# Performance work log

Hardware: AMD Instinct MI355X
Metric: run time of the kernel (lower is better)

The kernel has to match this reference:

```python
import jax, jax.numpy as jnp
import numpy as np

B, S, D, H = 4, 1024, 1024, 16
E = 8                 # num_experts
FF1 = 4096            # d_hidden * expansion_factor * 2 (swiglu in)
FF2 = 2048            # d_hidden * expansion_factor (swiglu out / linear2 in)
TEMP = 0.5            # gating temperature
RMS_EPS_GATE = float(np.finfo(np.float32).eps)  # torch RMSNorm default eps
NORM_EPS = 1e-8       # layer_norm_eps


def setup_inputs() -> dict:
    key = jax.random.key(0)
    ks = jax.random.split(key, 8)
    s = 0.02
    return {
        "x": jax.random.normal(ks[0], (B, S, D), jnp.float32),
        "w_qkv": jax.random.normal(ks[1], (3 * D, D), jnp.float32) * s,
        "w_out": jax.random.normal(ks[2], (D, D), jnp.float32) * s,
        "norm1_w": jnp.ones((D,), jnp.float32),
        "norm2_w": jnp.ones((D,), jnp.float32),
        "gate_w": jax.random.normal(ks[3], (E, D), jnp.float32) * s,
        "gate_b": jnp.zeros((E,), jnp.float32),
        "gate_rms_w": jnp.ones((E,), jnp.float32),
        "w1": jax.random.normal(ks[4], (E, D, FF1), jnp.float32) * s,
        "w2": jax.random.normal(ks[5], (E, FF2, D), jnp.float32) * s,
    }


def _rmsnorm(x, w, eps):
    return x * w * jax.lax.rsqrt(jnp.mean(x * x, axis=-1, keepdims=True) + eps)


def _attn(h, w_qkv, w_out):
    qkv = h @ w_qkv.T                              # [B,S,3D]
    q, k, v = jnp.split(qkv, 3, axis=-1)
    dh = D // H
    q = q.reshape(B, S, H, dh)
    k = k.reshape(B, S, H, dh)
    v = v.reshape(B, S, H, dh)
    scores = jnp.einsum("bqhd,bkhd->bhqk", q, k) / jnp.sqrt(jnp.float32(dh))
    p = jax.nn.softmax(scores, axis=-1)
    o = jnp.einsum("bhqk,bkhd->bqhd", p, v).reshape(B, S, D)
    return o @ w_out.T


def _moe(h, gate_w, gate_b, gate_rms_w, w1, w2):
    xf = h.reshape(-1, D)                          # [N,D]
    logits = _rmsnorm(xf @ gate_w.T + gate_b, gate_rms_w, RMS_EPS_GATE)
    gates = jax.nn.softmax(logits / TEMP, axis=-1)  # [N,E]
    top_g, _ = jax.lax.top_k(gates, 1)              # top_k = 1
    # capacity dispatch mask degenerates to all-ones (capacity >= 1), so
    # normalized gate = g / (g + 1e-6)
    g = top_g[:, 0] / (top_g[:, 0] + 1e-6)          # [N]
    h1 = jnp.einsum("nd,edf->nef", xf, w1)          # [N,E,FF1]
    a, b = jnp.split(h1, 2, axis=-1)                # SwiGLU
    act = a * jax.nn.silu(b)                        # [N,E,FF2]
    outs = jnp.einsum("nef,efd->ned", act, w2)      # [N,E,D]
    # gate broadcasts over the expert axis (as in the original code)
    comb = outs.sum(axis=1) * g[:, None]
    return comb.reshape(h.shape)


def reference(x, w_qkv, w_out, norm1_w, norm2_w, gate_w, gate_b, gate_rms_w, w1, w2):
    # pre-norm transformer block, eval mode (no dropout / gating noise)
    x = x + _attn(_rmsnorm(x, norm1_w, NORM_EPS), w_qkv, w_out)
    x = x + _moe(_rmsnorm(x, norm2_w, NORM_EPS), gate_w, gate_b, gate_rms_w, w1, w2)
    return x
```

## Files before the change

kernel.cpp:

```cpp
#include <hip/hip_runtime.h>
#include <hip/hip_bf16.h>
#include <math.h>

typedef __bf16 bf16_t;
typedef __bf16 bf16x8 __attribute__((ext_vector_type(8)));
typedef float f32x4 __attribute__((ext_vector_type(4)));

typedef const __attribute__((address_space(1))) void* gptr_t;
typedef __attribute__((address_space(3))) void* lptr_t;

#define MFMA16(a, b, c) __builtin_amdgcn_mfma_f32_16x16x32_bf16((a), (b), (c), 0, 0, 0)
#define BAR() __builtin_amdgcn_s_barrier()
#define WAIT_LGKM()                                        \
  do {                                                     \
    asm volatile("s_waitcnt lgkmcnt(0)" ::: "memory");     \
    __builtin_amdgcn_sched_barrier(0);                     \
  } while (0)
#define WAIT_VM4()                                         \
  do {                                                     \
    asm volatile("s_waitcnt vmcnt(4)" ::: "memory");       \
    __builtin_amdgcn_sched_barrier(0);                     \
  } while (0)
#define WAIT_VM8()                                         \
  do {                                                     \
    asm volatile("s_waitcnt vmcnt(8)" ::: "memory");       \
    __builtin_amdgcn_sched_barrier(0);                     \
  } while (0)
#define WAIT_VM0()                                         \
  do {                                                     \
    asm volatile("s_waitcnt vmcnt(0)" ::: "memory");       \
    __builtin_amdgcn_sched_barrier(0);                     \
  } while (0)

__device__ __forceinline__ void gload_lds16(const bf16_t* g, bf16_t* l) {
  __builtin_amdgcn_global_load_lds((gptr_t)g, (lptr_t)l, 16, 0, 0);
}

__global__ __launch_bounds__(256) void conv_kernel(const float* __restrict__ in,
                                                   bf16_t* __restrict__ out, int n4) {
  int i = blockIdx.x * 256 + threadIdx.x;
  if (i >= n4) return;
  float4 v = ((const float4*)in)[i];
  bf16_t* o = out + (size_t)i * 4;
  o[0] = (bf16_t)v.x; o[1] = (bf16_t)v.y; o[2] = (bf16_t)v.z; o[3] = (bf16_t)v.w;
}

__global__ __launch_bounds__(256) void transp_w1(const float* __restrict__ in,
                                                 bf16_t* __restrict__ out) {
  __shared__ float tile[32][33];
  const float* ip = in + (size_t)blockIdx.z * 1024 * 4096;
  bf16_t* op = out + (size_t)blockIdx.z * 4096 * 1024;
  int tx = threadIdx.x, ty = threadIdx.y;
  int r0 = blockIdx.y * 32, c0 = blockIdx.x * 32;
#pragma unroll
  for (int i = 0; i < 32; i += 8)
    tile[ty + i][tx] = ip[(size_t)(r0 + ty + i) * 4096 + c0 + tx];
  __syncthreads();
#pragma unroll
  for (int i = 0; i < 32; i += 8) {
    int c = c0 + ty + i;
    int p = (c < 2048) ? ((c >> 5) * 64 + (c & 31))
                       : (((c - 2048) >> 5) * 64 + 32 + ((c - 2048) & 31));
    op[(size_t)p * 1024 + r0 + tx] = (bf16_t)tile[tx][ty + i];
  }
}

__global__ __launch_bounds__(256) void transp_w2(const float* __restrict__ in,
                                                 bf16_t* __restrict__ out) {
  __shared__ float tile[32][33];
  const float* ip = in + (size_t)blockIdx.z * 2048 * 1024;
  int tx = threadIdx.x, ty = threadIdx.y;
  int r0 = blockIdx.y * 32, c0 = blockIdx.x * 32;
#pragma unroll
  for (int i = 0; i < 32; i += 8)
    tile[ty + i][tx] = ip[(size_t)(r0 + ty + i) * 1024 + c0 + tx];
  __syncthreads();
#pragma unroll
  for (int i = 0; i < 32; i += 8)
    out[(size_t)(c0 + ty + i) * 16384 + blockIdx.z * 2048 + r0 + tx] = (bf16_t)tile[tx][ty + i];
}

__global__ __launch_bounds__(256) void rmsnorm_kernel(const float* __restrict__ x,
                                                      const float* __restrict__ w,
                                                      bf16_t* __restrict__ out, float eps) {
  int row = blockIdx.x;
  int t = threadIdx.x;
  const float4* xr = (const float4*)(x + (size_t)row * 1024);
  float4 v = xr[t];
  float ss = v.x * v.x + v.y * v.y + v.z * v.z + v.w * v.w;
#pragma unroll
  for (int off = 1; off < 64; off <<= 1) ss += __shfl_xor(ss, off, 64);
  __shared__ float red[4];
  int wave = t >> 6, lane = t & 63;
  if (lane == 0) red[wave] = ss;
  __syncthreads();
  ss = red[0] + red[1] + red[2] + red[3];
  float inv = rsqrtf(ss * (1.0f / 1024.0f) + eps);
  float4 wv = ((const float4*)w)[t];
  bf16_t* o = out + (size_t)row * 1024 + t * 4;
  o[0] = (bf16_t)(v.x * wv.x * inv);
  o[1] = (bf16_t)(v.y * wv.y * inv);
  o[2] = (bf16_t)(v.z * wv.z * inv);
  o[3] = (bf16_t)(v.w * wv.w * inv);
}

template <int EPI>
__global__ __launch_bounds__(512, 2) void gemm256(const bf16_t* __restrict__ A,
                                                  const bf16_t* __restrict__ Bt,
                                                  void* __restrict__ C,
                                                  const float* __restrict__ resid,
                                                  int M, int N, int K, int lda, int ldb) {
  __shared__ bf16_t As[2][256 * 64];
  __shared__ bf16_t Bs[2][256 * 64];
  const int tid = threadIdx.x;
  const int wave = tid >> 6, lane = tid & 63;

  const int gx = gridDim.x, gy = gridDim.y;
  int nwg = gx * gy * gridDim.z;
  int lin = blockIdx.x + gx * (blockIdx.y + gy * blockIdx.z);
  int wid = ((nwg & 7) == 0) ? ((lin & 7) * (nwg >> 3) + (lin >> 3)) : lin;
  const int bx = wid % gx;
  const int by = (wid / gx) % gy;
  const int bz = wid / (gx * gy);

  const int m0 = by * 256, n0 = bx * 256;
  const int wr = (wave >> 2) * 128, wc = (wave & 3) * 64;
  const int fr = lane & 15, fq = lane >> 4;

  if (EPI == 4) Bt += (size_t)bz * 4096 * 1024;
  if (EPI == 5) {
    A += (size_t)bz * K;
    Bt += (size_t)bz * K;
  }

  const int srw = lane >> 3;
  const int sgc = (lane & 7) ^ srw;
  const bf16_t* aBase = A + (size_t)(m0 + wave * 8 + srw) * lda + sgc * 8;
  const bf16_t* bBase = Bt + (size_t)(n0 + wave * 8 + srw) * ldb + sgc * 8;

  auto stageA = [&](bf16_t* buf, int kt) {
#pragma unroll
    for (int i = 0; i < 4; ++i) {
      int r = i * 64;
      gload_lds16(aBase + (size_t)r * lda + kt * 64, &buf[(r + wave * 8) * 64]);
    }
  };
  auto stageB = [&](bf16_t* buf, int kt) {
#pragma unroll
    for (int i = 0; i < 4; ++i) {
      int r = i * 64;
      gload_lds16(bBase + (size_t)r * ldb + kt * 64, &buf[(r + wave * 8) * 64]);
    }
  };

  f32x4 acc[8][4] = {};
  bf16x8 a_[4][2], b_[4][2];

  auto readA = [&](int b, int mh) {
#pragma unroll
    for (int q = 0; q < 4; ++q)
#pragma unroll
      for (int ks = 0; ks < 2; ++ks) {
        int r = wr + mh * 64 + q * 16 + fr;
        a_[q][ks] = *(const bf16x8*)&As[b][r * 64 + (((fq + ks * 4) ^ (fr & 7)) << 3)];
      }
  };
  auto readB = [&](int b, int nh) {
#pragma unroll
    for (int q = 0; q < 2; ++q)
#pragma unroll
      for (int ks = 0; ks < 2; ++ks) {
        int r = wc + nh * 32 + q * 16 + fr;
        b_[nh * 2 + q][ks] = *(const bf16x8*)&Bs[b][r * 64 + (((fq + ks * 4) ^ (fr & 7)) << 3)];
      }
  };
  auto mfma16x = [&](int mh, int nh) {
    __builtin_amdgcn_s_setprio(1);
#pragma unroll
    for (int q = 0; q < 4; ++q)
#pragma unroll
      for (int n = 0; n < 2; ++n)
#pragma unroll
        for (int ks = 0; ks < 2; ++ks)
          acc[mh * 4 + q][nh * 2 + n] =
              MFMA16(a_[q][ks], b_[nh * 2 + n][ks], acc[mh * 4 + q][nh * 2 + n]);
    __builtin_amdgcn_s_setprio(0);
  };

  const int NKT = K >> 6;
  stageB(Bs[0], 0);
  stageA(As[0], 0);
  stageB(Bs[1], 1);
  stageA(As[1], 1);
  WAIT_VM8();
  BAR();
  readA(0, 0);
  readB(0, 0);

  for (int it = 0; it < (NKT >> 1) - 1; ++it) {
    const int t2 = 2 * it + 2, t3 = 2 * it + 3;
    WAIT_LGKM(); mfma16x(0, 0); readB(0, 1); BAR();
    WAIT_LGKM(); mfma16x(0, 1); readA(0, 1); BAR();
    WAIT_LGKM(); mfma16x(1, 0); stageB(Bs[0], t2); WAIT_VM4(); BAR();
    WAIT_LGKM(); mfma16x(1, 1); readA(1, 0); readB(1, 0); stageA(As[0], t2); BAR();
    WAIT_LGKM(); mfma16x(0, 0); readB(1, 1); BAR();
    WAIT_LGKM(); mfma16x(0, 1); readA(1, 1); BAR();
    WAIT_LGKM(); mfma16x(1, 0); stageB(Bs[1], t3); WAIT_VM4(); BAR();
    WAIT_LGKM(); mfma16x(1, 1); readA(0, 0); readB(0, 0); stageA(As[1], t3); BAR();
  }

  WAIT_LGKM(); mfma16x(0, 0); readB(0, 1); BAR();
  WAIT_LGKM(); mfma16x(0, 1); readA(0, 1); BAR();
  WAIT_LGKM(); mfma16x(1, 0); WAIT_VM0(); BAR();
  WAIT_LGKM(); mfma16x(1, 1); readA(1, 0); readB(1, 0); BAR();
  WAIT_LGKM(); mfma16x(0, 0); readB(1, 1); BAR();
  WAIT_LGKM(); mfma16x(0, 1); readA(1, 1); BAR();
  WAIT_LGKM(); mfma16x(1, 0); BAR();
  WAIT_LGKM(); mfma16x(1, 1);

  if (EPI == 4) {
    bf16_t* act = (bf16_t*)C;
    int strip = (n0 >> 6) + (wave & 3);
#pragma unroll
    for (int mq = 0; mq < 8; ++mq)
#pragma unroll
      for (int n = 0; n < 2; ++n)
#pragma unroll
        for (int j = 0; j < 4; ++j) {
          size_t row = (size_t)(m0 + wr + mq * 16 + fq * 4 + j);
          size_t col = (size_t)bz * 2048 + strip * 32 + n * 16 + fr;
          float a = acc[mq][n][j], b = acc[mq][n + 2][j];
          act[row * 16384 + col] = (bf16_t)(a * (b / (1.0f + __expf(-b))));
        }
    return;
  }
#pragma unroll
  for (int mq = 0; mq < 8; ++mq)
#pragma unroll
    for (int n = 0; n < 4; ++n)
#pragma unroll
      for (int j = 0; j < 4; ++j) {
        size_t row = (size_t)(m0 + wr + mq * 16 + fq * 4 + j);
        size_t col = (size_t)(n0 + wc + n * 16 + fr);
        float v = acc[mq][n][j];
        if (EPI == 0)
          ((bf16_t*)C)[row * N + col] = (bf16_t)v;
        else if (EPI == 1)
          ((float*)C)[row * N + col] = resid[row * N + col] + v;
        else if (EPI == 5)
          ((float*)C + (size_t)bz * M * N)[row * N + col] = v;
      }
}

__global__ __launch_bounds__(256) void attn_kernel(const bf16_t* __restrict__ qkv,
                                                   bf16_t* __restrict__ o) {
  const int S = 1024, LD = 3072;
  int qt = blockIdx.x, bh = blockIdx.y;
  int b = bh >> 4, h = bh & 15;
  int tid = threadIdx.x, wave = tid >> 6, lane = tid & 63;
  int fr = lane & 15, fq = lane >> 4, kg = fq * 8;
  int q0 = qt * 64 + wave * 16;
  const bf16_t* qb = qkv + (size_t)b * S * LD + h * 64;
  const bf16_t* kb = qb + 1024;
  const bf16_t* vb = qb + 2048;

  __shared__ bf16_t Ks[64 * 64];
  __shared__ bf16_t Vt[64 * 64];
  __shared__ bf16_t Ps[4][16 * 72];

  bf16x8 qf0 = *(const bf16x8*)&qb[(size_t)(q0 + fr) * LD + kg];
  bf16x8 qf1 = *(const bf16x8*)&qb[(size_t)(q0 + fr) * LD + 32 + kg];

  f32x4 acc[4] = {};
  float mrow[4] = {-1e30f, -1e30f, -1e30f, -1e30f};
  float ssum[4] = {0.f, 0.f, 0.f, 0.f};

  for (int k0 = 0; k0 < S; k0 += 64) {
#pragma unroll
    for (int cc = 0; cc < 2; ++cc) {
      int c = tid + cc * 256;
      int r = c >> 3, ch = c & 7;
      *(bf16x8*)&Ks[r * 64 + ((ch ^ (r & 7)) << 3)] =
          *(const bf16x8*)&kb[(size_t)(k0 + r) * LD + ch * 8];
      bf16x8 vv = *(const bf16x8*)&vb[(size_t)(k0 + r) * LD + ch * 8];
#pragma unroll
      for (int i = 0; i < 8; ++i) {
        int d = ch * 8 + i;
        int cs = ((r >> 3) ^ (d >> 3) ^ (d & 7)) & 7;
        Vt[d * 64 + cs * 8 + (r & 7)] = vv[i];
      }
    }
    __syncthreads();

    f32x4 s[4];
#pragma unroll
    for (int kc = 0; kc < 4; ++kc) {
      int row = kc * 16 + fr, sw = row & 7;
      bf16x8 kf0 = *(const bf16x8*)&Ks[row * 64 + ((fq ^ sw) << 3)];
      bf16x8 kf1 = *(const bf16x8*)&Ks[row * 64 + (((4 + fq) ^ sw) << 3)];
      f32x4 z = {};
      z = MFMA16(qf0, kf0, z);
      z = MFMA16(qf1, kf1, z);
      s[kc] = z * 0.125f;
    }
    float pmax[4], psum[4], scl[4];
#pragma unroll
    for (int j = 0; j < 4; ++j)
      pmax[j] = fmaxf(fmaxf(s[0][j], s[1][j]), fmaxf(s[2][j], s[3][j]));
#pragma unroll
    for (int off = 1; off < 16; off <<= 1)
#pragma unroll
      for (int j = 0; j < 4; ++j) pmax[j] = fmaxf(pmax[j], __shfl_xor(pmax[j], off, 64));
#pragma unroll
    for (int j = 0; j < 4; ++j) {
      float nm = fmaxf(mrow[j], pmax[j]);
      scl[j] = __expf(mrow[j] - nm);
      mrow[j] = nm;
      psum[j] = 0.f;
    }
#pragma unroll
    for (int kc = 0; kc < 4; ++kc)
#pragma unroll
      for (int j = 0; j < 4; ++j) {
        float p = __expf(s[kc][j] - mrow[j]);
        psum[j] += p;
        Ps[wave][(fq * 4 + j) * 72 + kc * 16 + fr] = (bf16_t)p;
      }
#pragma unroll
    for (int off = 1; off < 16; off <<= 1)
#pragma unroll
      for (int j = 0; j < 4; ++j) psum[j] += __shfl_xor(psum[j], off, 64);
#pragma unroll
    for (int j = 0; j < 4; ++j) ssum[j] = ssum[j] * scl[j] + psum[j];
#pragma unroll
    for (int n = 0; n < 4; ++n)
#pragma unroll
      for (int j = 0; j < 4; ++j) acc[n][j] *= scl[j];
    asm volatile("s_waitcnt lgkmcnt(0)" ::: "memory");
    bf16x8 pa[2];
#pragma unroll
    for (int ks = 0; ks < 2; ++ks) pa[ks] = *(const bf16x8*)&Ps[wave][fr * 72 + ks * 32 + kg];
#pragma unroll
    for (int n = 0; n < 4; ++n) {
      int d = n * 16 + fr;
      int swd = ((d >> 3) ^ (d & 7)) & 7;
#pragma unroll
      for (int ks = 0; ks < 2; ++ks) {
        bf16x8 vbf = *(const bf16x8*)&Vt[d * 64 + (((ks * 4 + fq) ^ swd) << 3)];
        acc[n] = MFMA16(pa[ks], vbf, acc[n]);
      }
    }
    __syncthreads();
  }
#pragma unroll
  for (int n = 0; n < 4; ++n)
#pragma unroll
    for (int j = 0; j < 4; ++j) {
      size_t row = (size_t)b * S + q0 + fq * 4 + j;
      o[row * 1024 + h * 64 + n * 16 + fr] = (bf16_t)(acc[n][j] / ssum[j]);
    }
}

__global__ __launch_bounds__(256) void gate_kernel(const bf16_t* __restrict__ hn,
                                                   const float* __restrict__ gw,
                                                   const float* __restrict__ gb,
                                                   const float* __restrict__ grms,
                                                   float* __restrict__ g) {
  int n = blockIdx.x * 4 + (threadIdx.x >> 6);
  int lane = threadIdx.x & 63;
  const bf16_t* xr = hn + (size_t)n * 1024;
  float acc[8] = {};
  for (int i = lane; i < 1024; i += 64) {
    float xv = (float)xr[i];
#pragma unroll
    for (int e = 0; e < 8; ++e) acc[e] += xv * gw[e * 1024 + i];
  }
#pragma unroll
  for (int e = 0; e < 8; ++e)
    for (int off = 1; off < 64; off <<= 1) acc[e] += __shfl_xor(acc[e], off, 64);
  float l[8], ms = 0.f;
#pragma unroll
  for (int e = 0; e < 8; ++e) {
    l[e] = acc[e] + gb[e];
    ms += l[e] * l[e];
  }
  float inv = rsqrtf(ms * 0.125f + 1.1920928955078125e-07f);
  float mx = -1e30f;
#pragma unroll
  for (int e = 0; e < 8; ++e) {
    l[e] = l[e] * inv * grms[e] * 2.0f;
    mx = fmaxf(mx, l[e]);
  }
  float s = 0.f;
#pragma unroll
  for (int e = 0; e < 8; ++e) s += __expf(l[e] - mx);
  float t = 1.0f / s;
  if (lane == 0) g[n] = t / (t + 1e-6f);
}

__global__ __launch_bounds__(256) void combine4(const float* __restrict__ moep,
                                                const float* __restrict__ x1,
                                                const float* __restrict__ g,
                                                float* __restrict__ out, int Mc) {
  size_t i4 = (size_t)blockIdx.x * 256 + threadIdx.x;
  size_t row = i4 >> 8;
  size_t stride4 = (size_t)Mc * 256;
  float4 s = {0.f, 0.f, 0.f, 0.f};
#pragma unroll
  for (int z = 0; z < 4; ++z) {
    float4 v = ((const float4*)moep)[z * stride4 + i4];
    s.x += v.x; s.y += v.y; s.z += v.z; s.w += v.w;
  }
  float gv = g[row];
  float4 xv = ((const float4*)x1)[i4];
  float4 r;
  r.x = xv.x + s.x * gv;
  r.y = xv.y + s.y * gv;
  r.z = xv.z + s.z * gv;
  r.w = xv.w + s.w * gv;
  ((float4*)out)[i4] = r;
}

extern "C" void kernel_launch(void* const* d_in, const int* in_sizes, int n_in,
                              void* d_out, int out_size, void* d_ws, size_t ws_size,
                              hipStream_t stream) {
  const float* x = (const float*)d_in[0];
  const float* w_qkv = (const float*)d_in[1];
  const float* w_out = (const float*)d_in[2];
  const float* norm1_w = (const float*)d_in[3];
  const float* norm2_w = (const float*)d_in[4];
  const float* gate_w = (const float*)d_in[5];
  const float* gate_b = (const float*)d_in[6];
  const float* gate_rms = (const float*)d_in[7];
  const float* w1 = (const float*)d_in[8];
  const float* w2 = (const float*)d_in[9];
  float* out = (float*)d_out;

  const size_t baseB = (8ull * 4096 * 1024 + 1024ull * 16384 + 3072ull * 1024 +
                        1024ull * 1024 + 4096ull * 1024) * 2 +
                       4096ull * 1024 * 4 + 4096 * 4;
  int cc = 4;
  if (ws_size >= baseB + 4096ull * 16384 * 2 + 4ull * 4096 * 1024 * 4)
    cc = 1;
  else if (ws_size >= baseB + 2048ull * 16384 * 2 + 4ull * 2048 * 1024 * 4)
    cc = 2;
  const int Mc = 4096 / cc;

  char* ws = (char*)d_ws;
  size_t off = 0;
  auto alloc = [&](size_t bytes) {
    char* p = ws + off;
    off += bytes;
    return p;
  };
  bf16_t* w1t = (bf16_t*)alloc(8ull * 4096 * 1024 * 2);
  bf16_t* w2t = (bf16_t*)alloc(1024ull * 16384 * 2);
  bf16_t* wqkvb = (bf16_t*)alloc(3072ull * 1024 * 2);
  bf16_t* woutb = (bf16_t*)alloc(1024ull * 1024 * 2);
  bf16_t* hn = (bf16_t*)alloc(4096ull * 1024 * 2);
  float* x1 = (float*)alloc(4096ull * 1024 * 4);
  float* gbuf = (float*)alloc(4096ull * 4);
  bf16_t* act = (bf16_t*)alloc((size_t)Mc * 16384 * 2);
  float* moep = (float*)alloc(4ull * Mc * 1024 * 4);
  bf16_t* qkvb = (bf16_t*)act;
  bf16_t* attno = (bf16_t*)moep;

  conv_kernel<<<3072, 256, 0, stream>>>(w_qkv, wqkvb, 3072 * 1024 / 4);
  conv_kernel<<<1024, 256, 0, stream>>>(w_out, woutb, 1024 * 1024 / 4);
  transp_w1<<<dim3(128, 32, 8), dim3(32, 8), 0, stream>>>(w1, w1t);
  transp_w2<<<dim3(32, 64, 8), dim3(32, 8), 0, stream>>>(w2, w2t);

  rmsnorm_kernel<<<4096, 256, 0, stream>>>(x, norm1_w, hn, 1e-8f);
  gemm256<0><<<dim3(12, 16), 512, 0, stream>>>(hn, wqkvb, qkvb, nullptr, 4096, 3072, 1024,
                                               1024, 1024);
  attn_kernel<<<dim3(16, 64), 256, 0, stream>>>(qkvb, attno);
  gemm256<1><<<dim3(4, 16), 512, 0, stream>>>(attno, woutb, x1, x, 4096, 1024, 1024, 1024,
                                              1024);

  rmsnorm_kernel<<<4096, 256, 0, stream>>>(x1, norm2_w, hn, 1e-8f);
  gate_kernel<<<1024, 256, 0, stream>>>(hn, gate_w, gate_b, gate_rms, gbuf);
  for (int c = 0; c < cc; ++c) {
    gemm256<4><<<dim3(16, Mc / 256, 8), 512, 0, stream>>>(
        hn + (size_t)c * Mc * 1024, w1t, act, nullptr, Mc, 4096, 1024, 1024, 1024);
    gemm256<5><<<dim3(4, Mc / 256, 4), 512, 0, stream>>>(
        act, w2t, moep, nullptr, Mc, 1024, 4096, 16384, 16384);
    combine4<<<Mc, 256, 0, stream>>>(moep, x1 + (size_t)c * Mc * 1024, gbuf + (size_t)c * Mc,
                                     out + (size_t)c * Mc * 1024, Mc);
  }
}
```

Measured before the change: 604.9 us.

## Restructure GEMM main loop into four phases with fewer barriers

Reorganizes the software-pipelined GEMM inner loop from eight barrier-separated phases to four. Each phase now issues two MFMA groups back to back, and s_setprio is raised around the combined group. Both B sub-tiles are read up front, and the A/B global stages are issued together with a vmcnt(8) wait. The aim is to cut barrier and lgkm wait overhead and to give longer uninterrupted MFMA bursts. In exchange, more LDS fragment reads are in flight at once, which raises register pressure, and load-compute interleaving becomes coarser.

```diff
diff --git a/kernel.cpp b/kernel.cpp
--- a/kernel.cpp
+++ b/kernel.cpp
@@ -14,11 +14,6 @@
 #define WAIT_LGKM()                                        \
   do {                                                     \
     asm volatile("s_waitcnt lgkmcnt(0)" ::: "memory");     \
-    __builtin_amdgcn_sched_barrier(0);                     \
-  } while (0)
-#define WAIT_VM4()                                         \
-  do {                                                     \
-    asm volatile("s_waitcnt vmcnt(4)" ::: "memory");       \
     __builtin_amdgcn_sched_barrier(0);                     \
   } while (0)
 #define WAIT_VM8()                                         \
@@ -175,7 +170,6 @@
       }
   };
   auto mfma16x = [&](int mh, int nh) {
-    __builtin_amdgcn_s_setprio(1);
 #pragma unroll
     for (int q = 0; q < 4; ++q)
 #pragma unroll
@@ -184,7 +178,6 @@
         for (int ks = 0; ks < 2; ++ks)
           acc[mh * 4 + q][nh * 2 + n] =
               MFMA16(a_[q][ks], b_[nh * 2 + n][ks], acc[mh * 4 + q][nh * 2 + n]);
-    __builtin_amdgcn_s_setprio(0);
   };
 
   const int NKT = K >> 6;
@@ -196,27 +189,71 @@
   BAR();
   readA(0, 0);
   readB(0, 0);
+  readB(0, 1);
 
   for (int it = 0; it < (NKT >> 1) - 1; ++it) {
     const int t2 = 2 * it + 2, t3 = 2 * it + 3;
-    WAIT_LGKM(); mfma16x(0, 0); readB(0, 1); BAR();
-    WAIT_LGKM(); mfma16x(0, 1); readA(0, 1); BAR();
-    WAIT_LGKM(); mfma16x(1, 0); stageB(Bs[0], t2); WAIT_VM4(); BAR();
-    WAIT_LGKM(); mfma16x(1, 1); readA(1, 0); readB(1, 0); stageA(As[0], t2); BAR();
-    WAIT_LGKM(); mfma16x(0, 0); readB(1, 1); BAR();
-    WAIT_LGKM(); mfma16x(0, 1); readA(1, 1); BAR();
-    WAIT_LGKM(); mfma16x(1, 0); stageB(Bs[1], t3); WAIT_VM4(); BAR();
-    WAIT_LGKM(); mfma16x(1, 1); readA(0, 0); readB(0, 0); stageA(As[1], t3); BAR();
-  }
-
-  WAIT_LGKM(); mfma16x(0, 0); readB(0, 1); BAR();
-  WAIT_LGKM(); mfma16x(0, 1); readA(0, 1); BAR();
-  WAIT_LGKM(); mfma16x(1, 0); WAIT_VM0(); BAR();
-  WAIT_LGKM(); mfma16x(1, 1); readA(1, 0); readB(1, 0); BAR();
-  WAIT_LGKM(); mfma16x(0, 0); readB(1, 1); BAR();
-  WAIT_LGKM(); mfma16x(0, 1); readA(1, 1); BAR();
-  WAIT_LGKM(); mfma16x(1, 0); BAR();
-  WAIT_LGKM(); mfma16x(1, 1);
+    WAIT_LGKM();
+    __builtin_amdgcn_s_setprio(1);
+    mfma16x(0, 0); mfma16x(0, 1);
+    __builtin_amdgcn_s_setprio(0);
+    readA(0, 1);
+    BAR();
+    WAIT_LGKM();
+    __builtin_amdgcn_s_setprio(1);
+    mfma16x(1, 0); mfma16x(1, 1);
+    __builtin_amdgcn_s_setprio(0);
+    stageB(Bs[0], t2);
+    stageA(As[0], t2);
+    WAIT_VM8();
+    readA(1, 0);
+    readB(1, 0);
+    readB(1, 1);
+    BAR();
+    WAIT_LGKM();
+    __builtin_amdgcn_s_setprio(1);
+    mfma16x(0, 0); mfma16x(0, 1);
+    __builtin_amdgcn_s_setprio(0);
+    readA(1, 1);
+    BAR();
+    WAIT_LGKM();
+    __builtin_amdgcn_s_setprio(1);
+    mfma16x(1, 0); mfma16x(1, 1);
+    __builtin_amdgcn_s_setprio(0);
+    stageB(Bs[1], t3);
+    stageA(As[1], t3);
+    WAIT_VM8();
+    readA(0, 0);
+    readB(0, 0);
+    readB(0, 1);
+    BAR();
+  }
+
+  WAIT_LGKM();
+  __builtin_amdgcn_s_setprio(1);
+  mfma16x(0, 0); mfma16x(0, 1);
+  __builtin_amdgcn_s_setprio(0);
+  readA(0, 1);
+  BAR();
+  WAIT_LGKM();
+  __builtin_amdgcn_s_setprio(1);
+  mfma16x(1, 0); mfma16x(1, 1);
+  __builtin_amdgcn_s_setprio(0);
+  WAIT_VM0();
+  readA(1, 0);
+  readB(1, 0);
+  readB(1, 1);
+  BAR();
+  WAIT_LGKM();
+  __builtin_amdgcn_s_setprio(1);
+  mfma16x(0, 0); mfma16x(0, 1);
+  __builtin_amdgcn_s_setprio(0);
+  readA(1, 1);
+  BAR();
+  WAIT_LGKM();
+  __builtin_amdgcn_s_setprio(1);
+  mfma16x(1, 0); mfma16x(1, 1);
+  __builtin_amdgcn_s_setprio(0);
 
   if (EPI == 4) {
     bf16_t* act = (bf16_t*)C;
```

After: 757.0 us. 1.25x slower.
